# Kernel optimization log

Measured on AMD Instinct MI355X. Metric: run time of the kernel, lower is better.

Reference implementation:

```python
import jax, jax.numpy as jnp
import numpy as np

EPS = 1e-12  # matches torch F.normalize default eps in spectral_norm


def _l2norm(v):
    return v / jnp.maximum(jnp.linalg.norm(v), EPS)


def _spectral_norm(W, u):
    # One power-iteration step (torch spectral_norm training behavior).
    # u, v are treated as constants w.r.t. gradients.
    v = jax.lax.stop_gradient(_l2norm(W.T @ u))
    u2 = jax.lax.stop_gradient(_l2norm(W @ v))
    sigma = jnp.einsum('o,oi,i->', u2, W, v)
    return W / sigma


def setup_inputs() -> dict:
    key = jax.random.key(0)
    ks = jax.random.split(key, 8)
    B, C, N = 8, 512, 2048
    d = C // 8
    return {
        'x':  jax.random.normal(ks[0], (B, C, N), dtype=jnp.float32),
        'Wq': jax.random.normal(ks[1], (d, C), dtype=jnp.float32) * (1.0 / np.sqrt(C)),
        'Wk': jax.random.normal(ks[2], (d, C), dtype=jnp.float32) * (1.0 / np.sqrt(C)),
        'Wv': jax.random.normal(ks[3], (C, C), dtype=jnp.float32) * (1.0 / np.sqrt(C)),
        'uq': jax.random.normal(ks[4], (d,), dtype=jnp.float32),
        'uk': jax.random.normal(ks[5], (d,), dtype=jnp.float32),
        'uv': jax.random.normal(ks[6], (C,), dtype=jnp.float32),
        'gamma': jax.random.normal(ks[7], (1,), dtype=jnp.float32) * 0.1,
    }


def reference(x, Wq, Wk, Wv, uq, uk, uv, gamma):
    # x: [B, C, N]
    f = jnp.einsum('oi,bin->bon', _spectral_norm(Wq, uq), x)  # [B, C/8, N]
    g = jnp.einsum('oi,bin->bon', _spectral_norm(Wk, uk), x)  # [B, C/8, N]
    h = jnp.einsum('oi,bin->bon', _spectral_norm(Wv, uv), x)  # [B, C, N]
    scores = jnp.einsum('bdn,bdm->bnm', f, g)                 # f^T g: [B, N, N]
    beta = jax.nn.softmax(scores, axis=1)                      # softmax over dim=1
    o = gamma[0] * jnp.einsum('bcn,bnm->bcm', h, beta) + x    # [B, C, N]
    return o
```

## Files before the change

kernel.cpp:

```cpp
#include <hip/hip_runtime.h>
#include <hip/hip_bf16.h>
#include <math.h>

#define B_ 8
#define C_ 512
#define N_ 2048
#define D_ 64
#define O_ 640

typedef __bf16 bf16x8 __attribute__((ext_vector_type(8)));
typedef float f32x4 __attribute__((ext_vector_type(4)));
typedef unsigned short ushort8_t __attribute__((ext_vector_type(8)));
typedef unsigned short ushort4_t __attribute__((ext_vector_type(4)));

__device__ __forceinline__ unsigned short f2bf(float f) {
    unsigned int u = __builtin_bit_cast(unsigned int, f);
    u += 0x7fffu + ((u >> 16) & 1u);
    return (unsigned short)(u >> 16);
}

__device__ __forceinline__ float fastexp(float x) {
    return exp2f(x * 1.44269504088896340736f);
}

union FragU { ushort8_t u; bf16x8 b; };

__device__ __forceinline__ bf16x8 ldfrag(const unsigned short* p) {
    FragU t; t.u = *(const ushort8_t*)p; return t.b;
}

__device__ __forceinline__ void gload_lds16(const unsigned short* g, unsigned short* l) {
    __builtin_amdgcn_global_load_lds((const __attribute__((address_space(1))) void*)g,
                                     (__attribute__((address_space(3))) void*)l,
                                     16, 0, 0);
}

__global__ __launch_bounds__(512) void k_colvec(const float* __restrict__ Wq,
                                                const float* __restrict__ Wk,
                                                const float* __restrict__ Wv,
                                                const float* __restrict__ uq,
                                                const float* __restrict__ uk,
                                                const float* __restrict__ uv,
                                                float* __restrict__ tpart) {
    int which = blockIdx.y, oq = blockIdx.x;
    const float* W; const float* u; int R;
    if (which == 0)      { W = Wq; u = uq; R = 64;  }
    else if (which == 1) { W = Wk; u = uk; R = 64;  }
    else                 { W = Wv; u = uv; R = 512; }
    int chunk = R >> 2;
    int i = threadIdx.x;
    float s = 0.f;
    int o0 = oq * chunk, o1 = o0 + chunk;
    for (int o = o0; o < o1; ++o) s += W[(size_t)o * 512 + i] * u[o];
    tpart[((which << 2) + oq) * 512 + i] = s;
}

__global__ __launch_bounds__(512) void k_trow(const float* __restrict__ tpart,
                                              float* __restrict__ tvec,
                                              float* __restrict__ t2) {
    int which = blockIdx.x, i = threadIdx.x;
    const float* tp = tpart + (which << 2) * 512;
    float s = tp[i] + tp[512 + i] + tp[1024 + i] + tp[1536 + i];
    tvec[which * 512 + i] = s;
    __shared__ float red[512];
    red[i] = s * s; __syncthreads();
    for (int st = 256; st > 0; st >>= 1) { if (i < st) red[i] += red[i + st]; __syncthreads(); }
    if (i == 0) t2[which] = red[0];
}

__global__ __launch_bounds__(256) void k_rowvec(const float* __restrict__ Wq,
                                                const float* __restrict__ Wk,
                                                const float* __restrict__ Wv,
                                                const float* __restrict__ tvec,
                                                float* __restrict__ wpart) {
    int which = blockIdx.y;
    const float* W; int R;
    if (which == 0)      { W = Wq; R = 64;  }
    else if (which == 1) { W = Wk; R = 64;  }
    else                 { W = Wv; R = 512; }
    int tid = threadIdx.x, lane = tid & 63, wv = tid >> 6;
    int row = blockIdx.x * 4 + wv;
    float ps = 0.f;
    if (row < R) {
        const float4* wr_ = (const float4*)(W + (size_t)row * 512);
        const float4* tv = (const float4*)(tvec + which * 512);
        float4 a0 = wr_[lane * 2], a1 = wr_[lane * 2 + 1];
        float4 b0 = tv[lane * 2], b1 = tv[lane * 2 + 1];
        float s = a0.x * b0.x + a0.y * b0.y + a0.z * b0.z + a0.w * b0.w
                + a1.x * b1.x + a1.y * b1.y + a1.z * b1.z + a1.w * b1.w;
        #pragma unroll
        for (int off = 1; off < 64; off <<= 1) s += __shfl_xor(s, off, 64);
        ps = s * s;
    }
    __shared__ float red[4];
    if (lane == 0) red[wv] = ps;
    __syncthreads();
    if (tid == 0) wpart[which * 128 + blockIdx.x] = red[0] + red[1] + red[2] + red[3];
}

__global__ __launch_bounds__(128) void k_scale(const float* __restrict__ wpart,
                                               const float* __restrict__ t2,
                                               float* __restrict__ scales) {
    int which = blockIdx.x, tid = threadIdx.x;
    float s = wpart[which * 128 + tid];
    #pragma unroll
    for (int off = 1; off < 64; off <<= 1) s += __shfl_xor(s, off, 64);
    __shared__ float r2[2];
    if ((tid & 63) == 0) r2[tid >> 6] = s;
    __syncthreads();
    if (tid == 0) scales[which] = sqrtf(t2[which] / fmaxf(r2[0] + r2[1], 1e-24f));
}

__global__ __launch_bounds__(256) void k_wconv(const float* __restrict__ Wq,
                                               const float* __restrict__ Wk,
                                               const float* __restrict__ Wv,
                                               const float* __restrict__ scales,
                                               unsigned short* __restrict__ Wb) {
    int gid = blockIdx.x * 256 + threadIdx.x;
    int e0 = gid * 8;
    int o = e0 >> 9, i = e0 & 511;
    const float* src; float sc;
    if (o < 64)       { src = Wq + (size_t)o * 512;         sc = scales[0]; }
    else if (o < 128) { src = Wk + (size_t)(o - 64) * 512;  sc = scales[1]; }
    else              { src = Wv + (size_t)(o - 128) * 512; sc = scales[2]; }
    float4 v0 = *(const float4*)(src + i), v1 = *(const float4*)(src + i + 4);
    ushort8_t u;
    u[0] = f2bf(v0.x * sc); u[1] = f2bf(v0.y * sc); u[2] = f2bf(v0.z * sc); u[3] = f2bf(v0.w * sc);
    u[4] = f2bf(v1.x * sc); u[5] = f2bf(v1.y * sc); u[6] = f2bf(v1.z * sc); u[7] = f2bf(v1.w * sc);
    *(ushort8_t*)&Wb[(size_t)o * 512 + i] = u;
}

__global__ __launch_bounds__(256) void k_transpose(const float* __restrict__ x,
                                                   unsigned short* __restrict__ xT) {
    __shared__ float tile[64][33];
    int b = blockIdx.z;
    int n0 = blockIdx.x * 32, c0 = blockIdx.y * 64;
    int tx = threadIdx.x, ty = threadIdx.y;
    #pragma unroll
    for (int k = 0; k < 8; ++k) {
        int c = ty + k * 8;
        tile[c][tx] = x[((size_t)b * C_ + c0 + c) * N_ + n0 + tx];
    }
    __syncthreads();
    #pragma unroll
    for (int k = 0; k < 4; ++k) {
        int n = ty + k * 8;
        unsigned int p = (unsigned int)f2bf(tile[tx * 2][n]) |
                         ((unsigned int)f2bf(tile[tx * 2 + 1][n]) << 16);
        *(unsigned int*)&xT[((size_t)b * N_ + n0 + n) * C_ + c0 + tx * 2] = p;
    }
}

__global__ __launch_bounds__(256) void k_proj(const unsigned short* __restrict__ xT,
                                              const unsigned short* __restrict__ Wb,
                                              unsigned short* __restrict__ fT,
                                              unsigned short* __restrict__ gT,
                                              unsigned short* __restrict__ hb) {
    int b = blockIdx.z, n0 = blockIdx.y * 128, o0 = blockIdx.x * 128;
    int tid = threadIdx.x, lane = tid & 63, w = tid >> 6;
    int wr = w >> 1, wc = w & 1;
    __shared__ __align__(16) unsigned short Sh[16384];
    unsigned short* As = Sh;
    unsigned short* Bs = Sh + 8192;
    f32x4 zero = {0.f, 0.f, 0.f, 0.f};
    f32x4 acc[4][4];
    #pragma unroll
    for (int i = 0; i < 4; ++i)
        #pragma unroll
        for (int j = 0; j < 4; ++j) acc[i][j] = zero;
    int r8 = lane >> 3, s = lane & 7;
    int scol = (s ^ r8) * 8;

    for (int kt = 0; kt < 8; ++kt) {
        #pragma unroll
        for (int q = 0; q < 4; ++q) {
            int chunk = w * 4 + q;
            int row = chunk * 8 + r8;
            gload_lds16(xT + ((size_t)b * N_ + n0 + row) * C_ + kt * 64 + scol, &As[chunk * 512]);
            gload_lds16(Wb + (size_t)(o0 + row) * C_ + kt * 64 + scol, &Bs[chunk * 512]);
        }
        __syncthreads();
        int kg = lane >> 4, r16 = lane & 15;
        #pragma unroll
        for (int kk = 0; kk < 2; ++kk) {
            int sw = kk * 4 + kg;
            bf16x8 af[4];
            #pragma unroll
            for (int i = 0; i < 4; ++i) {
                int row = wr * 64 + i * 16 + r16;
                af[i] = ldfrag(&As[row * 64 + (sw ^ (row & 7)) * 8]);
            }
            #pragma unroll
            for (int j = 0; j < 4; ++j) {
                int row = wc * 64 + j * 16 + r16;
                bf16x8 bv = ldfrag(&Bs[row * 64 + (sw ^ (row & 7)) * 8]);
                #pragma unroll
                for (int i = 0; i < 4; ++i)
                    acc[i][j] = __builtin_amdgcn_mfma_f32_16x16x32_bf16(af[i], bv, acc[i][j], 0, 0, 0);
            }
        }
        __syncthreads();
    }

    unsigned short* St = Sh;
    if (o0 == 0) {
        #pragma unroll
        for (int p = 0; p < 2; ++p) {
            if (wc == p) {
                #pragma unroll
                for (int i = 0; i < 4; ++i)
                    #pragma unroll
                    for (int j = 0; j < 4; ++j)
                        #pragma unroll
                        for (int r = 0; r < 4; ++r)
                            St[(wr * 64 + i * 16 + (lane >> 4) * 4 + r) * 72 + j * 16 + (lane & 15)] = f2bf(acc[i][j][r]);
            }
            __syncthreads();
            unsigned short* dst = p == 0 ? fT : gT;
            #pragma unroll
            for (int it = 0; it < 4; ++it) {
                int row = it * 32 + (tid >> 3);
                *(ushort8_t*)&dst[((size_t)b * N_ + n0 + row) * D_ + (tid & 7) * 8] =
                    *(ushort8_t*)&St[row * 72 + (tid & 7) * 8];
            }
            __syncthreads();
        }
    } else {
        int ho0 = o0 - 128;
        #pragma unroll
        for (int p = 0; p < 2; ++p) {
            if (wc == p) {
                #pragma unroll
                for (int i = 0; i < 4; ++i)
                    #pragma unroll
                    for (int j = 0; j < 4; ++j)
                        #pragma unroll
                        for (int r = 0; r < 4; ++r)
                            St[(j * 16 + (lane & 15)) * 136 + wr * 64 + i * 16 + (lane >> 4) * 4 + r] = f2bf(acc[i][j][r]);
            }
            __syncthreads();
            #pragma unroll
            for (int it = 0; it < 4; ++it) {
                int row = it * 16 + (tid >> 4);
                *(ushort8_t*)&hb[((size_t)b * C_ + ho0 + p * 64 + row) * N_ + n0 + (tid & 15) * 8] =
                    *(ushort8_t*)&St[row * 136 + (tid & 15) * 8];
            }
            __syncthreads();
        }
    }
}

__global__ __launch_bounds__(256) void k_stats(const unsigned short* __restrict__ fT,
                                               const unsigned short* __restrict__ gT,
                                               float* __restrict__ colmax,
                                               float* __restrict__ colsinv) {
    int b = blockIdx.y, m0 = blockIdx.x * 16;
    int tid = threadIdx.x, lane = tid & 63, w = tid >> 6;
    int mcol = m0 + (lane & 15);
    const unsigned short* gbase = gT + ((size_t)b * N_ + mcol) * D_ + (lane >> 4) * 8;
    bf16x8 g0 = ldfrag(gbase);
    bf16x8 g1 = ldfrag(gbase + 32);

    float mx = -1e30f, sm = 0.f;
    for (int nt = w * 32; nt < w * 32 + 32; ++nt) {
        const unsigned short* abase = fT + ((size_t)b * N_ + nt * 16 + (lane & 15)) * D_ + (lane >> 4) * 8;
        f32x4 s = {0.f, 0.f, 0.f, 0.f};
        s = __builtin_amdgcn_mfma_f32_16x16x32_bf16(ldfrag(abase), g0, s, 0, 0, 0);
        s = __builtin_amdgcn_mfma_f32_16x16x32_bf16(ldfrag(abase + 32), g1, s, 0, 0, 0);
        float tm = fmaxf(fmaxf(s[0], s[1]), fmaxf(s[2], s[3]));
        float nm = fmaxf(mx, tm);
        float c = fastexp(mx - nm);
        sm = sm * c + fastexp(s[0] - nm) + fastexp(s[1] - nm) + fastexp(s[2] - nm) + fastexp(s[3] - nm);
        mx = nm;
    }
    #pragma unroll
    for (int off = 16; off < 64; off <<= 1) {
        float omx = __shfl_xor(mx, off, 64);
        float osm = __shfl_xor(sm, off, 64);
        float nm = fmaxf(mx, omx);
        sm = sm * fastexp(mx - nm) + osm * fastexp(omx - nm);
        mx = nm;
    }
    __shared__ float lmx[4][16], lsm[4][16];
    if ((lane >> 4) == 0) { lmx[w][lane & 15] = mx; lsm[w][lane & 15] = sm; }
    __syncthreads();
    if (tid < 16) {
        float M = lmx[0][tid], S = lsm[0][tid];
        #pragma unroll
        for (int q = 1; q < 4; ++q) {
            float om = lmx[q][tid], os = lsm[q][tid];
            float nm = fmaxf(M, om);
            S = S * fastexp(M - nm) + os * fastexp(om - nm);
            M = nm;
        }
        colmax[(size_t)b * N_ + m0 + tid] = M;
        colsinv[(size_t)b * N_ + m0 + tid] = 1.0f / S;
    }
}

__global__ __launch_bounds__(512) void k_av(const unsigned short* __restrict__ fT,
                                            const unsigned short* __restrict__ gT,
                                            const unsigned short* __restrict__ hb,
                                            const float* __restrict__ colmax,
                                            const float* __restrict__ colsinv,
                                            const float* __restrict__ x,
                                            const float* __restrict__ gamma,
                                            float* __restrict__ out) {
    __shared__ __align__(16) unsigned short FT[2][4096];
    __shared__ __align__(16) unsigned short HB[2][16384];
    __shared__ __align__(16) unsigned short BS[8192];

    int bid = blockIdx.x;
    int xg = bid & 7, sidx = bid >> 3;
    int bc = xg + 8 * (sidx >> 4);
    int mi = sidx & 15;
    int b = bc >> 1, ch = bc & 1;
    int m0 = mi * 128, c0 = ch * 256;

    int tid = threadIdx.x, lane = tid & 63, w = tid >> 6;
    int nw = w & 3, mh = w >> 2;
    int l15 = lane & 15, lq = lane >> 4;
    int r8 = lane >> 3, sl = lane & 7;
    int scol = (sl ^ r8) * 8;

    bf16x8 gf[4][2];
    float mx_[4], siv_[4];
    #pragma unroll
    for (int j = 0; j < 4; ++j) {
        int m = m0 + mh * 64 + j * 16 + l15;
        #pragma unroll
        for (int kd = 0; kd < 2; ++kd)
            gf[j][kd] = ldfrag(gT + ((size_t)b * N_ + m) * D_ + kd * 32 + lq * 8);
        mx_[j] = colmax[(size_t)b * N_ + m];
        siv_[j] = colsinv[(size_t)b * N_ + m];
    }

    f32x4 zero = {0.f, 0.f, 0.f, 0.f};
    f32x4 acc[4][4];
    #pragma unroll
    for (int i = 0; i < 4; ++i)
        #pragma unroll
        for (int j = 0; j < 4; ++j) acc[i][j] = zero;

    const unsigned short* fbase = fT + ((size_t)b * N_) * D_;
    const unsigned short* hbase = hb + ((size_t)b * C_ + c0) * N_;

    {
        int frow = w * 8 + r8;
        gload_lds16(fbase + (size_t)frow * D_ + scol, &FT[0][w * 512]);
        #pragma unroll
        for (int q = 0; q < 4; ++q) {
            int ci = w * 4 + q;
            int crow = ci * 8 + r8;
            gload_lds16(hbase + (size_t)crow * N_ + scol, &HB[0][ci * 512]);
        }
    }

    int buf = 0;
    for (int kt = 0; kt < N_ / 64; ++kt) {
        __syncthreads();

        int arow = nw * 16 + l15;
        bf16x8 af0 = ldfrag(&FT[buf][arow * 64 + ((lq ^ (arow & 7)) * 8)]);
        bf16x8 af1 = ldfrag(&FT[buf][arow * 64 + (((4 + lq) ^ (arow & 7)) * 8)]);
        #pragma unroll
        for (int j = 0; j < 4; ++j) {
            f32x4 sv = zero;
            sv = __builtin_amdgcn_mfma_f32_16x16x32_bf16(af0, gf[j][0], sv, 0, 0, 0);
            sv = __builtin_amdgcn_mfma_f32_16x16x32_bf16(af1, gf[j][1], sv, 0, 0, 0);
            int mrel = mh * 64 + j * 16 + l15;
            ushort4_t pk;
            #pragma unroll
            for (int r = 0; r < 4; ++r)
                pk[r] = f2bf(fastexp(sv[r] - mx_[j]) * siv_[j]);
            int nt = nw * 16 + lq * 4;
            *(ushort4_t*)&BS[mrel * 64 + (((nt >> 3) ^ (mrel & 7)) * 8) + (nt & 7)] = pk;
        }
        __syncthreads();

        if (kt + 1 < N_ / 64) {
            int nb = buf ^ 1;
            int frow = w * 8 + r8;
            gload_lds16(fbase + ((size_t)(kt + 1) * 64 + frow) * D_ + scol, &FT[nb][w * 512]);
            #pragma unroll
            for (int q = 0; q < 4; ++q) {
                int ci = w * 4 + q;
                int crow = ci * 8 + r8;
                gload_lds16(hbase + (size_t)crow * N_ + (kt + 1) * 64 + scol, &HB[nb][ci * 512]);
            }
        }

        #pragma unroll
        for (int kk = 0; kk < 2; ++kk) {
            int ng = kk * 4 + lq;
            bf16x8 pa[4];
            #pragma unroll
            for (int i = 0; i < 4; ++i) {
                int mr = mh * 64 + i * 16 + l15;
                pa[i] = ldfrag(&BS[mr * 64 + ((ng ^ (mr & 7)) * 8)]);
            }
            #pragma unroll
            for (int j = 0; j < 4; ++j) {
                int cr = nw * 64 + j * 16 + l15;
                bf16x8 hv = ldfrag(&HB[buf][cr * 64 + ((ng ^ (cr & 7)) * 8)]);
                #pragma unroll
                for (int i = 0; i < 4; ++i)
                    acc[i][j] = __builtin_amdgcn_mfma_f32_16x16x32_bf16(pa[i], hv, acc[i][j], 0, 0, 0);
            }
        }
        buf ^= 1;
    }

    float gv = gamma[0];
    #pragma unroll
    for (int i = 0; i < 4; ++i) {
        int mabs = m0 + mh * 64 + i * 16 + lq * 4;
        #pragma unroll
        for (int j = 0; j < 4; ++j) {
            int cabs = c0 + nw * 64 + j * 16 + l15;
            size_t base = ((size_t)b * C_ + cabs) * N_ + mabs;
            float4 xv = *(const float4*)(x + base);
            float4 ov;
            ov.x = gv * acc[i][j][0] + xv.x;
            ov.y = gv * acc[i][j][1] + xv.y;
            ov.z = gv * acc[i][j][2] + xv.z;
            ov.w = gv * acc[i][j][3] + xv.w;
            *(float4*)(out + base) = ov;
        }
    }
}

extern "C" void kernel_launch(void* const* d_in, const int* in_sizes, int n_in,
                              void* d_out, int out_size, void* d_ws, size_t ws_size,
                              hipStream_t stream) {
    const float* x     = (const float*)d_in[0];
    const float* Wq    = (const float*)d_in[1];
    const float* Wk    = (const float*)d_in[2];
    const float* Wv    = (const float*)d_in[3];
    const float* uq    = (const float*)d_in[4];
    const float* uk    = (const float*)d_in[5];
    const float* uv    = (const float*)d_in[6];
    const float* gamma = (const float*)d_in[7];
    float* out = (float*)d_out;

    char* wsb = (char*)d_ws;
    float* scales         = (float*)wsb;
    unsigned short* xT    = (unsigned short*)(wsb + 256);
    unsigned short* fT    = xT + (size_t)B_ * N_ * C_;
    unsigned short* gT    = fT + (size_t)B_ * N_ * D_;
    unsigned short* hb    = gT + (size_t)B_ * N_ * D_;
    float* colmax         = (float*)(hb + (size_t)B_ * C_ * N_);
    float* colsinv        = colmax + (size_t)B_ * N_;
    float* tpart          = colsinv + (size_t)B_ * N_;
    float* tvec           = tpart + 3 * 4 * 512;
    float* t2             = tvec + 3 * 512;
    float* wpart          = t2 + 16;
    unsigned short* Wb    = (unsigned short*)(wpart + 3 * 128);

    k_colvec<<<dim3(4, 3), 512, 0, stream>>>(Wq, Wk, Wv, uq, uk, uv, tpart);
    k_trow<<<3, 512, 0, stream>>>(tpart, tvec, t2);
    k_rowvec<<<dim3(128, 3), 256, 0, stream>>>(Wq, Wk, Wv, tvec, wpart);
    k_scale<<<3, 128, 0, stream>>>(wpart, t2, scales);
    k_wconv<<<O_ * C_ / (256 * 8), 256, 0, stream>>>(Wq, Wk, Wv, scales, Wb);
    k_transpose<<<dim3(N_ / 32, C_ / 64, B_), dim3(32, 8), 0, stream>>>(x, xT);
    k_proj<<<dim3(O_ / 128, N_ / 128, B_), 256, 0, stream>>>(xT, Wb, fT, gT, hb);
    k_stats<<<dim3(N_ / 16, B_), 256, 0, stream>>>(fT, gT, colmax, colsinv);
    k_av<<<256, 512, 0, stream>>>(fT, gT, hb, colmax, colsinv, x, gamma, out);
}
```

Before: 186.5 us.

## Split k_av channel tile to 128 to double grid and add MFMA priority

Each k_av block now covers 128 channels instead of 256, so the grid doubles from 256 to 512 blocks, HB shared-memory staging is halved and the accumulator set shrinks. Launch bounds now request 4 blocks per CU, s_setprio raises wave priority around the MFMA loop, and the bf16 conversion of softmax probabilities uses the hardware cast. The aim is more occupancy and more blocks on a 256-CU part. The cost is that every score tile (QK^T MFMA plus exp) is recomputed twice as often across channel groups.

New measurement: 192.0 us. 3.0% more time.

```diff
diff --git a/kernel.cpp b/kernel.cpp
--- a/kernel.cpp
+++ b/kernel.cpp
@@ -17,6 +17,11 @@
     unsigned int u = __builtin_bit_cast(unsigned int, f);
     u += 0x7fffu + ((u >> 16) & 1u);
     return (unsigned short)(u >> 16);
+}
+
+__device__ __forceinline__ unsigned short f2bf_hw(float f) {
+    __bf16 h = (__bf16)f;
+    return __builtin_bit_cast(unsigned short, h);
 }
 
 __device__ __forceinline__ float fastexp(float x) {
@@ -298,24 +303,24 @@
     }
 }
 
-__global__ __launch_bounds__(512) void k_av(const unsigned short* __restrict__ fT,
-                                            const unsigned short* __restrict__ gT,
-                                            const unsigned short* __restrict__ hb,
-                                            const float* __restrict__ colmax,
-                                            const float* __restrict__ colsinv,
-                                            const float* __restrict__ x,
-                                            const float* __restrict__ gamma,
-                                            float* __restrict__ out) {
+__global__ __launch_bounds__(512, 4) void k_av(const unsigned short* __restrict__ fT,
+                                               const unsigned short* __restrict__ gT,
+                                               const unsigned short* __restrict__ hb,
+                                               const float* __restrict__ colmax,
+                                               const float* __restrict__ colsinv,
+                                               const float* __restrict__ x,
+                                               const float* __restrict__ gamma,
+                                               float* __restrict__ out) {
     __shared__ __align__(16) unsigned short FT[2][4096];
-    __shared__ __align__(16) unsigned short HB[2][16384];
+    __shared__ __align__(16) unsigned short HB[2][8192];
     __shared__ __align__(16) unsigned short BS[8192];
 
     int bid = blockIdx.x;
     int xg = bid & 7, sidx = bid >> 3;
-    int bc = xg + 8 * (sidx >> 4);
-    int mi = sidx & 15;
-    int b = bc >> 1, ch = bc & 1;
-    int m0 = mi * 128, c0 = ch * 256;
+    int mi = sidx & 15, gh = sidx >> 4;
+    int g = xg + 8 * gh;
+    int b = g >> 2, cq = g & 3;
+    int m0 = mi * 128, c0 = cq * 128;
 
     int tid = threadIdx.x, lane = tid & 63, w = tid >> 6;
     int nw = w & 3, mh = w >> 2;
@@ -336,23 +341,21 @@
     }
 
     f32x4 zero = {0.f, 0.f, 0.f, 0.f};
-    f32x4 acc[4][4];
+    f32x4 acc[4][2];
     #pragma unroll
     for (int i = 0; i < 4; ++i)
         #pragma unroll
-        for (int j = 0; j < 4; ++j) acc[i][j] = zero;
+        for (int j = 0; j < 2; ++j) acc[i][j] = zero;
 
     const unsigned short* fbase = fT + ((size_t)b * N_) * D_;
     const unsigned short* hbase = hb + ((size_t)b * C_ + c0) * N_;
 
     {
-        int frow = w * 8 + r8;
-        gload_lds16(fbase + (size_t)frow * D_ + scol, &FT[0][w * 512]);
-        #pragma unroll
-        for (int q = 0; q < 4; ++q) {
-            int ci = w * 4 + q;
-            int crow = ci * 8 + r8;
-            gload_lds16(hbase + (size_t)crow * N_ + scol, &HB[0][ci * 512]);
+        gload_lds16(fbase + (size_t)(w * 8 + r8) * D_ + scol, &FT[0][w * 512]);
+        #pragma unroll
+        for (int q = 0; q < 2; ++q) {
+            int ci = w * 2 + q;
+            gload_lds16(hbase + (size_t)(ci * 8 + r8) * N_ + scol, &HB[0][ci * 512]);
         }
     }
 
@@ -372,7 +375,7 @@
             ushort4_t pk;
             #pragma unroll
             for (int r = 0; r < 4; ++r)
-                pk[r] = f2bf(fastexp(sv[r] - mx_[j]) * siv_[j]);
+                pk[r] = f2bf_hw(fastexp(sv[r] - mx_[j]) * siv_[j]);
             int nt = nw * 16 + lq * 4;
             *(ushort4_t*)&BS[mrel * 64 + (((nt >> 3) ^ (mrel & 7)) * 8) + (nt & 7)] = pk;
         }
@@ -380,16 +383,15 @@
 
         if (kt + 1 < N_ / 64) {
             int nb = buf ^ 1;
-            int frow = w * 8 + r8;
-            gload_lds16(fbase + ((size_t)(kt + 1) * 64 + frow) * D_ + scol, &FT[nb][w * 512]);
-            #pragma unroll
-            for (int q = 0; q < 4; ++q) {
-                int ci = w * 4 + q;
-                int crow = ci * 8 + r8;
-                gload_lds16(hbase + (size_t)crow * N_ + (kt + 1) * 64 + scol, &HB[nb][ci * 512]);
-            }
-        }
-
+            gload_lds16(fbase + ((size_t)(kt + 1) * 64 + w * 8 + r8) * D_ + scol, &FT[nb][w * 512]);
+            #pragma unroll
+            for (int q = 0; q < 2; ++q) {
+                int ci = w * 2 + q;
+                gload_lds16(hbase + (size_t)(ci * 8 + r8) * N_ + (kt + 1) * 64 + scol, &HB[nb][ci * 512]);
+            }
+        }
+
+        __builtin_amdgcn_s_setprio(1);
         #pragma unroll
         for (int kk = 0; kk < 2; ++kk) {
             int ng = kk * 4 + lq;
@@ -400,14 +402,15 @@
                 pa[i] = ldfrag(&BS[mr * 64 + ((ng ^ (mr & 7)) * 8)]);
             }
             #pragma unroll
-            for (int j = 0; j < 4; ++j) {
-                int cr = nw * 64 + j * 16 + l15;
+            for (int j = 0; j < 2; ++j) {
+                int cr = nw * 32 + j * 16 + l15;
                 bf16x8 hv = ldfrag(&HB[buf][cr * 64 + ((ng ^ (cr & 7)) * 8)]);
                 #pragma unroll
                 for (int i = 0; i < 4; ++i)
                     acc[i][j] = __builtin_amdgcn_mfma_f32_16x16x32_bf16(pa[i], hv, acc[i][j], 0, 0, 0);
             }
         }
+        __builtin_amdgcn_s_setprio(0);
         buf ^= 1;
     }
 
@@ -416,8 +419,8 @@
     for (int i = 0; i < 4; ++i) {
         int mabs = m0 + mh * 64 + i * 16 + lq * 4;
         #pragma unroll
-        for (int j = 0; j < 4; ++j) {
-            int cabs = c0 + nw * 64 + j * 16 + l15;
+        for (int j = 0; j < 2; ++j) {
+            int cabs = c0 + nw * 32 + j * 16 + l15;
             size_t base = ((size_t)b * C_ + cabs) * N_ + mabs;
             float4 xv = *(const float4*)(x + base);
             float4 ov;
@@ -465,5 +468,5 @@
     k_transpose<<<dim3(N_ / 32, C_ / 64, B_), dim3(32, 8), 0, stream>>>(x, xT);
     k_proj<<<dim3(O_ / 128, N_ / 128, B_), 256, 0, stream>>>(xT, Wb, fT, gT, hb);
     k_stats<<<dim3(N_ / 16, B_), 256, 0, stream>>>(fT, gT, colmax, colsinv);
-    k_av<<<256, 512, 0, stream>>>(fT, gT, hb, colmax, colsinv, x, gamma, out);
-}
+    k_av<<<512, 512, 0, stream>>>(fT, gT, hb, colmax, colsinv, x, gamma, out);
+}
```
